# Kernel tuning notes

Measured on AMD Instinct MI355X. Metric: run time of the kernel, lower is better.

Reference implementation:

```python
import jax, jax.numpy as jnp
import numpy as np

N_NODES = 10000
N_EDGES = 640000
NODE_DIM = 128
EDGE_DIM = 32
OUT_DIM = 128


def setup_inputs() -> dict:
    key = jax.random.key(0)
    k_h, k_e, k_ef, k_w1, k_w2 = jax.random.split(key, 5)
    h = jax.random.normal(k_h, (N_NODES, NODE_DIM), dtype=jnp.float32)
    edge_index = jax.random.randint(k_e, (2, N_EDGES), 0, N_NODES, dtype=jnp.int64)
    edge_features = jax.random.normal(k_ef, (N_EDGES, EDGE_DIM), dtype=jnp.float32)
    in_dim = 2 * NODE_DIM + EDGE_DIM
    # Kaiming-ish init scale for realism
    W1 = jax.random.normal(k_w1, (in_dim, OUT_DIM), dtype=jnp.float32) / np.sqrt(in_dim)
    b1 = jnp.zeros((OUT_DIM,), dtype=jnp.float32)
    W2 = jax.random.normal(k_w2, (OUT_DIM, OUT_DIM), dtype=jnp.float32) / np.sqrt(OUT_DIM)
    b2 = jnp.zeros((OUT_DIM,), dtype=jnp.float32)
    return {"h": h, "edge_index": edge_index, "edge_features": edge_features,
            "n": N_NODES, "W1": W1, "b1": b1, "W2": W2, "b2": b2}


def reference(h, edge_index, edge_features, n, W1, b1, W2, b2):
    rows, cols = edge_index[0], edge_index[1]
    # gather source/target node features + edge features -> [E, 2*node_dim+edge_dim]
    msg_input = jnp.concatenate([h[rows], h[cols], edge_features], axis=-1)
    hidden = jax.nn.relu(msg_input @ W1 + b1)   # [E, out_dim]
    messages = hidden @ W2 + b2                 # [E, out_dim]
    # scatter-add messages onto destination rows -> [n, out_dim]
    out = jax.ops.segment_sum(messages, rows, num_segments=n)
    return out
```

## Files before the change

kernel.cpp:

```cpp
#include <hip/hip_runtime.h>
#include <hip/hip_bf16.h>


typedef __attribute__((ext_vector_type(8))) short bf16x8;
typedef __attribute__((ext_vector_type(4))) float f32x4;

#define ND 128
#define ED 32
#define CH 64

__device__ __forceinline__ short f2bf(float x) {
  unsigned int u = __float_as_uint(x);
  unsigned int r = (u + 0x7FFFu + ((u >> 16) & 1u)) >> 16;
  return (short)r;
}

__device__ __forceinline__ float bf2f(short s) {
  return __uint_as_float(((unsigned int)(unsigned short)s) << 16);
}

__device__ __forceinline__ f32x4 bf8lo(bf16x8 v) {
  f32x4 r;
  #pragma unroll
  for (int j = 0; j < 4; ++j) r[j] = bf2f(v[j]);
  return r;
}
__device__ __forceinline__ f32x4 bf8hi(bf16x8 v) {
  f32x4 r;
  #pragma unroll
  for (int j = 0; j < 4; ++j) r[j] = bf2f(v[4 + j]);
  return r;
}

__device__ __forceinline__ int load_idx(const void* ei, long long i, int is64) {
  return is64 ? (int)((const long long*)ei)[i] : ((const int*)ei)[i];
}

__device__ __forceinline__ int swz(int c) {
  int ct = c >> 4, cc = c & 15;
  return (ct >> 2) * 64 + (cc >> 2) * 16 + (ct & 3) * 4 + (cc & 3);
}

__global__ __launch_bounds__(256) void prep_kernel(
    const float* __restrict__ W1, const float* __restrict__ W2,
    const unsigned int* __restrict__ ei, short* __restrict__ w12t,
    short* __restrict__ w1eA, short* __restrict__ w2t, int* __restrict__ flag,
    int* __restrict__ counts, int N) {
  if (blockIdx.x == 0 && threadIdx.x == 0) {
    int is64 = 1;
    for (int i = 0; i < 16; ++i)
      if (ei[2 * i + 1] != 0u) is64 = 0;
    flag[0] = is64;
  }
  int t = blockIdx.x * blockDim.x + threadIdx.x;
  for (int i = t; i < N; i += 32768) counts[i] = 0;
  if (t < 256 * 128) {
    int np = t >> 7, k = t & 127;
    float v = (np < 128) ? W1[k * 128 + np] : W1[(128 + k) * 128 + (np - 128)];
    w12t[t] = f2bf(v);
  }
  if (t < 128 * 128) {
    int n = t >> 7, k = t & 127;
    w2t[t] = f2bf(W2[k * 128 + n]);
  }
  if (t < 8 * 64 * 8) {
    int ct = t >> 9, lane = (t >> 3) & 63, j = t & 7;
    int li = lane & 15, lg = lane >> 4;
    w1eA[t] = f2bf(W1[(256 + lg * 8 + j) * 128 + ct * 16 + li]);
  }
}

__global__ void hist_kernel(const void* __restrict__ ei, const int* __restrict__ flag,
                            int* __restrict__ counts, int* __restrict__ rank,
                            unsigned int* __restrict__ rc, int E) {
  int e = blockIdx.x * blockDim.x + threadIdx.x;
  if (e >= E) return;
  int f = flag[0];
  int r = load_idx(ei, e, f);
  int c = load_idx(ei, (long long)E + e, f);
  rank[e] = atomicAdd(&counts[r], 1);
  rc[e] = ((unsigned int)r << 16) | (unsigned int)c;
}

__global__ __launch_bounds__(1024) void scan_kernel(const int* __restrict__ counts,
                                                    int* __restrict__ row_ptr, int n) {
  __shared__ int wtot[16];
  int tid = threadIdx.x;
  int lane = tid & 63, w = tid >> 6;
  int base_i = tid * 16;
  int c[16];
  int tot = 0;
  #pragma unroll
  for (int j = 0; j < 16; ++j) {
    int i = base_i + j;
    c[j] = (i < n) ? counts[i] : 0;
    tot += c[j];
  }
  int x = tot;
  #pragma unroll
  for (int d = 1; d < 64; d <<= 1) {
    int t = __shfl_up(x, d);
    if (lane >= d) x += t;
  }
  if (lane == 63) wtot[w] = x;
  __syncthreads();
  if (w == 0) {
    int y = (lane < 16) ? wtot[lane] : 0;
    #pragma unroll
    for (int d = 1; d < 16; d <<= 1) {
      int t = __shfl_up(y, d);
      if (lane >= d) y += t;
    }
    if (lane < 16) wtot[lane] = y;
  }
  __syncthreads();
  int waveoff = (w == 0) ? 0 : wtot[w - 1];
  int run = waveoff + x - tot;
  if (tid == 0) row_ptr[0] = 0;
  #pragma unroll
  for (int j = 0; j < 16; ++j) {
    int i = base_i + j;
    if (i < n) {
      run += c[j];
      row_ptr[i + 1] = run;
    }
  }
}

__global__ __launch_bounds__(256, 4) void scatter_sg_kernel(
    const float* __restrict__ ef, const int* __restrict__ row_ptr,
    const int* __restrict__ rank, const unsigned int* __restrict__ rc,
    const float* __restrict__ h, const short* __restrict__ w12t,
    const float* __restrict__ b1, short* __restrict__ efb,
    unsigned short* __restrict__ ccol, int2* __restrict__ cb,
    float* __restrict__ s2, short* __restrict__ g2, int N, int E, int nchunks) {
  int b = blockIdx.x;
  int SGB = (N + 63) >> 6;
  int SCB = (4 * E + 255) >> 8;
  if (b < SGB) {
    int lane = threadIdx.x & 63, w = threadIdx.x >> 6;
    int li = lane & 15, lg = lane >> 4;
    int base = b * 64 + w * 16;
    int rowm = base + li;
    if (rowm >= N) rowm = N - 1;
    float breg[8];
    #pragma unroll
    for (int nt = 0; nt < 8; ++nt) breg[nt] = b1[nt * 16 + li];
    f32x4 acc[16];
    #pragma unroll
    for (int nt = 0; nt < 16; ++nt) acc[nt] = (f32x4){0.f, 0.f, 0.f, 0.f};
    #pragma unroll
    for (int kc = 0; kc < 4; ++kc) {
      f32x4 f0 = *(const f32x4*)(h + (size_t)rowm * ND + kc * 32 + lg * 8);
      f32x4 f1 = *(const f32x4*)(h + (size_t)rowm * ND + kc * 32 + lg * 8 + 4);
      bf16x8 a;
      #pragma unroll
      for (int j = 0; j < 4; ++j) { a[j] = f2bf(f0[j]); a[4 + j] = f2bf(f1[j]); }
      #pragma unroll
      for (int nt = 0; nt < 16; ++nt) {
        bf16x8 bb = *(const bf16x8*)(w12t + (nt * 16 + li) * 128 + kc * 32 + lg * 8);
        acc[nt] = __builtin_amdgcn_mfma_f32_16x16x32_bf16(a, bb, acc[nt], 0, 0, 0);
      }
    }
    #pragma unroll
    for (int nt = 0; nt < 16; ++nt)
      #pragma unroll
      for (int r = 0; r < 4; ++r) {
        int row = base + lg * 4 + r;
        if (row < N) {
          if (nt < 8) {
            s2[(size_t)row * 128 + swz(nt * 16 + li)] = acc[nt][r] + breg[nt];
          } else {
            g2[(size_t)row * 128 + swz((nt - 8) * 16 + li)] = f2bf(acc[nt][r]);
          }
        }
      }
  } else if (b < SGB + SCB) {
    int gt = (b - SGB) * 256 + threadIdx.x;
    int e = gt >> 2, part = gt & 3;
    if (e < E) {
      unsigned int p = rc[e];
      int r = (int)(p >> 16), c = (int)(p & 0xffffu);
      int pos = row_ptr[r] + rank[e];
      f32x4 a0 = *(const f32x4*)(ef + (size_t)e * ED + part * 8);
      f32x4 a1 = *(const f32x4*)(ef + (size_t)e * ED + part * 8 + 4);
      bf16x8 ob;
      #pragma unroll
      for (int j = 0; j < 4; ++j) { ob[j] = f2bf(a0[j]); ob[4 + j] = f2bf(a1[j]); }
      *(bf16x8*)(efb + (size_t)pos * ED + part * 8) = ob;
      if (part == 0) ccol[pos] = (unsigned short)c;
    }
  } else {
    int k = (b - SGB - SCB) * 256 + threadIdx.x;
    if (k < nchunks) {
      int t0 = k * CH, t1 = t0 + CH;
      int lo = 0, hi = N;
      while (lo < hi) { int mid = (lo + hi) >> 1; if (row_ptr[mid] < t0) lo = mid + 1; else hi = mid; }
      int na = lo;
      hi = N;
      while (lo < hi) { int mid = (lo + hi) >> 1; if (row_ptr[mid] < t1) lo = mid + 1; else hi = mid; }
      cb[k] = make_int2(na, lo);
    }
  }
}

__global__ __launch_bounds__(128, 4) void layer1_kernel(
    const float* __restrict__ s2, const short* __restrict__ g2,
    const short* __restrict__ efb, const unsigned short* __restrict__ ccol,
    const short* __restrict__ w1eA, const int* __restrict__ row_ptr,
    const int2* __restrict__ cb, float* __restrict__ hsum) {
  int2 bounds = cb[blockIdx.x];
  int na = bounds.x, nb = bounds.y;
  if (na >= nb) return;
  int lane = threadIdx.x & 63;
  int w = threadIdx.x >> 6;
  int li = lane & 15, lg = lane >> 4;

  bf16x8 wa[4];
  #pragma unroll
  for (int nt = 0; nt < 4; ++nt)
    wa[nt] = *(const bf16x8*)(w1eA + ((w * 4 + nt) * 64 + lane) * 8);

  for (int n = na; n < nb; ++n) {
    int rp = row_ptr[n], rpe = row_ptr[n + 1];
    int deg = rpe - rp;
    f32x4 sreg[4];
    #pragma unroll
    for (int nt = 0; nt < 4; ++nt)
      sreg[nt] = *(const f32x4*)(s2 + (size_t)n * 128 + w * 64 + lg * 16 + nt * 4);
    f32x4 psum[4];
    #pragma unroll
    for (int nt = 0; nt < 4; ++nt) psum[nt] = (f32x4){0.f, 0.f, 0.f, 0.f};

    int ntiles = (deg + 15) >> 4;
    int last = rpe - 1;
    auto ldpos = [&](int t) {
      int p = rp + t * 16 + li;
      return p > last ? last : p;
    };

    int pA = ldpos(0), pB = ldpos(1);
    int cA = ccol[pA], cB = ccol[pB];
    bf16x8 eA = *(const bf16x8*)(efb + (size_t)pA * ED + lg * 8);
    bf16x8 eB = *(const bf16x8*)(efb + (size_t)pB * ED + lg * 8);
    const short* gpA = g2 + (size_t)cA * 128 + w * 64 + lg * 16;
    bf16x8 gA0 = *(const bf16x8*)gpA;
    bf16x8 gA1 = *(const bf16x8*)(gpA + 8);

    for (int t = 0; t < ntiles; ++t) {
      const short* gpB = g2 + (size_t)cB * 128 + w * 64 + lg * 16;
      bf16x8 gB0 = *(const bf16x8*)gpB;
      bf16x8 gB1 = *(const bf16x8*)(gpB + 8);
      int pC = ldpos(t + 2);
      int cC = ccol[pC];
      bf16x8 eC = *(const bf16x8*)(efb + (size_t)pC * ED + lg * 8);
      f32x4 a0 = __builtin_amdgcn_mfma_f32_16x16x32_bf16(wa[0], eA, (f32x4){0.f,0.f,0.f,0.f}, 0, 0, 0);
      f32x4 a1 = __builtin_amdgcn_mfma_f32_16x16x32_bf16(wa[1], eA, (f32x4){0.f,0.f,0.f,0.f}, 0, 0, 0);
      f32x4 a2 = __builtin_amdgcn_mfma_f32_16x16x32_bf16(wa[2], eA, (f32x4){0.f,0.f,0.f,0.f}, 0, 0, 0);
      f32x4 a3 = __builtin_amdgcn_mfma_f32_16x16x32_bf16(wa[3], eA, (f32x4){0.f,0.f,0.f,0.f}, 0, 0, 0);
      if ((t * 16 + li) < deg) {
        f32x4 v0 = a0 + sreg[0] + bf8lo(gA0);
        f32x4 v1 = a1 + sreg[1] + bf8hi(gA0);
        f32x4 v2 = a2 + sreg[2] + bf8lo(gA1);
        f32x4 v3 = a3 + sreg[3] + bf8hi(gA1);
        #pragma unroll
        for (int r = 0; r < 4; ++r) {
          psum[0][r] += (v0[r] > 0.f ? v0[r] : 0.f);
          psum[1][r] += (v1[r] > 0.f ? v1[r] : 0.f);
          psum[2][r] += (v2[r] > 0.f ? v2[r] : 0.f);
          psum[3][r] += (v3[r] > 0.f ? v3[r] : 0.f);
        }
      }
      cB = cC; eA = eB; eB = eC;
      gA0 = gB0; gA1 = gB1;
    }

    #pragma unroll
    for (int nt = 0; nt < 4; ++nt)
      #pragma unroll
      for (int r = 0; r < 4; ++r) {
        float v = psum[nt][r];
        v += __shfl_xor(v, 1);
        v += __shfl_xor(v, 2);
        v += __shfl_xor(v, 4);
        v += __shfl_xor(v, 8);
        psum[nt][r] = v;
      }
    if (li == 0) {
      #pragma unroll
      for (int nt = 0; nt < 4; ++nt)
        *(f32x4*)(hsum + (size_t)n * 128 + w * 64 + nt * 16 + lg * 4) = psum[nt];
    }
  }
}

__global__ __launch_bounds__(256) void out_kernel(const float* __restrict__ hsum,
                                                  const short* __restrict__ w2t,
                                                  const float* __restrict__ b2,
                                                  const int* __restrict__ row_ptr,
                                                  float* __restrict__ out, int N) {
  int lane = threadIdx.x & 63, w = threadIdx.x >> 6;
  int li = lane & 15, lg = lane >> 4;
  int base = blockIdx.x * 64 + w * 16;
  int rowm = base + li;
  if (rowm >= N) rowm = N - 1;
  float breg[8];
  #pragma unroll
  for (int nt = 0; nt < 8; ++nt) breg[nt] = b2[nt * 16 + li];
  f32x4 acc[8];
  #pragma unroll
  for (int nt = 0; nt < 8; ++nt) acc[nt] = (f32x4){0.f, 0.f, 0.f, 0.f};
  #pragma unroll
  for (int kc = 0; kc < 4; ++kc) {
    f32x4 f0 = *(const f32x4*)(hsum + (size_t)rowm * 128 + kc * 32 + lg * 8);
    f32x4 f1 = *(const f32x4*)(hsum + (size_t)rowm * 128 + kc * 32 + lg * 8 + 4);
    bf16x8 a;
    #pragma unroll
    for (int j = 0; j < 4; ++j) { a[j] = f2bf(f0[j]); a[4 + j] = f2bf(f1[j]); }
    #pragma unroll
    for (int nt = 0; nt < 8; ++nt) {
      bf16x8 bb = *(const bf16x8*)(w2t + (nt * 16 + li) * 128 + kc * 32 + lg * 8);
      acc[nt] = __builtin_amdgcn_mfma_f32_16x16x32_bf16(a, bb, acc[nt], 0, 0, 0);
    }
  }
  #pragma unroll
  for (int r = 0; r < 4; ++r) {
    int row = base + lg * 4 + r;
    if (row < N) {
      float dg = (float)(row_ptr[row + 1] - row_ptr[row]);
      #pragma unroll
      for (int nt = 0; nt < 8; ++nt)
        out[(size_t)row * 128 + nt * 16 + li] = acc[nt][r] + dg * breg[nt];
    }
  }
}

extern "C" void kernel_launch(void* const* d_in, const int* in_sizes, int n_in,
                              void* d_out, int out_size, void* d_ws, size_t ws_size,
                              hipStream_t stream) {
  const float* h  = (const float*)d_in[0];
  const void*  ei = d_in[1];
  const float* ef = (const float*)d_in[2];
  const float* W1 = (const float*)d_in[4];
  const float* b1 = (const float*)d_in[5];
  const float* W2 = (const float*)d_in[6];
  const float* b2 = (const float*)d_in[7];
  float* out = (float*)d_out;
  int N = in_sizes[0] / ND;
  int E = in_sizes[2] / ED;
  int nchunks = (E + CH - 1) / CH;

  char* ws = (char*)d_ws;
  size_t off = 0;
  auto alloc = [&](size_t bytes) {
    size_t o = off;
    off = (off + bytes + 255) & ~(size_t)255;
    return o;
  };
  int*            flag    = (int*)(ws + alloc(4));
  int*            counts  = (int*)(ws + alloc((size_t)N * 4));
  int*            row_ptr = (int*)(ws + alloc((size_t)(N + 1) * 4));
  int*            rank    = (int*)(ws + alloc((size_t)E * 4));
  unsigned int*   rc      = (unsigned int*)(ws + alloc((size_t)E * 4));
  short*          w12t    = (short*)(ws + alloc(256 * 128 * 2));
  short*          w1eA    = (short*)(ws + alloc(8 * 64 * 8 * 2));
  short*          w2t     = (short*)(ws + alloc(128 * 128 * 2));
  float*          s2      = (float*)(ws + alloc((size_t)N * 128 * 4));
  short*          g2      = (short*)(ws + alloc((size_t)N * 128 * 2));
  float*          hsumb   = (float*)(ws + alloc((size_t)N * 128 * 4));
  short*          efb     = (short*)(ws + alloc((size_t)E * ED * 2));
  unsigned short* ccol    = (unsigned short*)(ws + alloc((size_t)E * 2));
  int2*           cbb     = (int2*)(ws + alloc((size_t)nchunks * 8));

  int SGB = (N + 63) >> 6;
  int SCB = (4 * E + 255) >> 8;
  int CBB = (nchunks + 255) >> 8;

  prep_kernel<<<128, 256, 0, stream>>>(W1, W2, (const unsigned int*)ei, w12t, w1eA, w2t,
                                       flag, counts, N);
  hist_kernel<<<(E + 255) / 256, 256, 0, stream>>>(ei, flag, counts, rank, rc, E);
  scan_kernel<<<1, 1024, 0, stream>>>(counts, row_ptr, N);
  scatter_sg_kernel<<<SGB + SCB + CBB, 256, 0, stream>>>(
      ef, row_ptr, rank, rc, h, w12t, b1, efb, ccol, cbb, s2, g2, N, E, nchunks);
  layer1_kernel<<<nchunks, 128, 0, stream>>>(s2, g2, efb, ccol, w1eA, row_ptr, cbb, hsumb);
  out_kernel<<<(N + 63) / 64, 256, 0, stream>>>(hsumb, w2t, b2, row_ptr, out, N);
}
```

Measured before the change: 139.1 us.

## Assign one layer1 block per node instead of edge-balanced chunks

Replaces edge-chunked scheduling in layer1 with one workgroup per destination node. This removes the binary-search chunk-boundary pass and the per-block node loop. The column index array widens to 32-bit ints, and the hist kernel inlines its index-width branch. In exchange, load balance now depends on the degree distribution, and ccol traffic doubles.

```diff
diff --git a/kernel.cpp b/kernel.cpp
--- a/kernel.cpp
+++ b/kernel.cpp
@@ -7,7 +7,6 @@
 
 #define ND 128
 #define ED 32
-#define CH 64
 
 __device__ __forceinline__ short f2bf(float x) {
   unsigned int u = __float_as_uint(x);
@@ -30,10 +29,6 @@
   #pragma unroll
   for (int j = 0; j < 4; ++j) r[j] = bf2f(v[4 + j]);
   return r;
-}
-
-__device__ __forceinline__ int load_idx(const void* ei, long long i, int is64) {
-  return is64 ? (int)((const long long*)ei)[i] : ((const int*)ei)[i];
 }
 
 __device__ __forceinline__ int swz(int c) {
@@ -76,8 +71,14 @@
   int e = blockIdx.x * blockDim.x + threadIdx.x;
   if (e >= E) return;
   int f = flag[0];
-  int r = load_idx(ei, e, f);
-  int c = load_idx(ei, (long long)E + e, f);
+  int r, c;
+  if (f) {
+    r = (int)((const long long*)ei)[e];
+    c = (int)((const long long*)ei)[(long long)E + e];
+  } else {
+    r = ((const int*)ei)[e];
+    c = ((const int*)ei)[E + e];
+  }
   rank[e] = atomicAdd(&counts[r], 1);
   rc[e] = ((unsigned int)r << 16) | (unsigned int)c;
 }
@@ -132,11 +133,10 @@
     const int* __restrict__ rank, const unsigned int* __restrict__ rc,
     const float* __restrict__ h, const short* __restrict__ w12t,
     const float* __restrict__ b1, short* __restrict__ efb,
-    unsigned short* __restrict__ ccol, int2* __restrict__ cb,
-    float* __restrict__ s2, short* __restrict__ g2, int N, int E, int nchunks) {
+    int* __restrict__ ccol, float* __restrict__ s2, short* __restrict__ g2,
+    int N, int E) {
   int b = blockIdx.x;
   int SGB = (N + 63) >> 6;
-  int SCB = (4 * E + 255) >> 8;
   if (b < SGB) {
     int lane = threadIdx.x & 63, w = threadIdx.x >> 6;
     int li = lane & 15, lg = lane >> 4;
@@ -175,7 +175,7 @@
           }
         }
       }
-  } else if (b < SGB + SCB) {
+  } else {
     int gt = (b - SGB) * 256 + threadIdx.x;
     int e = gt >> 2, part = gt & 3;
     if (e < E) {
@@ -188,109 +188,103 @@
       #pragma unroll
       for (int j = 0; j < 4; ++j) { ob[j] = f2bf(a0[j]); ob[4 + j] = f2bf(a1[j]); }
       *(bf16x8*)(efb + (size_t)pos * ED + part * 8) = ob;
-      if (part == 0) ccol[pos] = (unsigned short)c;
-    }
-  } else {
-    int k = (b - SGB - SCB) * 256 + threadIdx.x;
-    if (k < nchunks) {
-      int t0 = k * CH, t1 = t0 + CH;
-      int lo = 0, hi = N;
-      while (lo < hi) { int mid = (lo + hi) >> 1; if (row_ptr[mid] < t0) lo = mid + 1; else hi = mid; }
-      int na = lo;
-      hi = N;
-      while (lo < hi) { int mid = (lo + hi) >> 1; if (row_ptr[mid] < t1) lo = mid + 1; else hi = mid; }
-      cb[k] = make_int2(na, lo);
+      if (part == 0) ccol[pos] = c;
     }
   }
 }
 
 __global__ __launch_bounds__(128, 4) void layer1_kernel(
     const float* __restrict__ s2, const short* __restrict__ g2,
-    const short* __restrict__ efb, const unsigned short* __restrict__ ccol,
+    const short* __restrict__ efb, const int* __restrict__ ccol,
     const short* __restrict__ w1eA, const int* __restrict__ row_ptr,
-    const int2* __restrict__ cb, float* __restrict__ hsum) {
-  int2 bounds = cb[blockIdx.x];
-  int na = bounds.x, nb = bounds.y;
-  if (na >= nb) return;
+    float* __restrict__ hsum) {
+  int node = blockIdx.x;
   int lane = threadIdx.x & 63;
   int w = threadIdx.x >> 6;
   int li = lane & 15, lg = lane >> 4;
+  int rp = row_ptr[node], rpe = row_ptr[node + 1];
+  int deg = rpe - rp;
+
+  if (deg == 0) {
+    if (li == 0) {
+      #pragma unroll
+      for (int nt = 0; nt < 4; ++nt)
+        *(f32x4*)(hsum + (size_t)node * 128 + w * 64 + nt * 16 + lg * 4) =
+            (f32x4){0.f, 0.f, 0.f, 0.f};
+    }
+    return;
+  }
 
   bf16x8 wa[4];
   #pragma unroll
   for (int nt = 0; nt < 4; ++nt)
     wa[nt] = *(const bf16x8*)(w1eA + ((w * 4 + nt) * 64 + lane) * 8);
-
-  for (int n = na; n < nb; ++n) {
-    int rp = row_ptr[n], rpe = row_ptr[n + 1];
-    int deg = rpe - rp;
-    f32x4 sreg[4];
+  f32x4 sreg[4];
+  #pragma unroll
+  for (int nt = 0; nt < 4; ++nt)
+    sreg[nt] = *(const f32x4*)(s2 + (size_t)node * 128 + w * 64 + lg * 16 + nt * 4);
+  f32x4 psum[4];
+  #pragma unroll
+  for (int nt = 0; nt < 4; ++nt) psum[nt] = (f32x4){0.f, 0.f, 0.f, 0.f};
+
+  int ntiles = (deg + 15) >> 4;
+  int last = rpe - 1;
+  auto ldpos = [&](int t) {
+    int p = rp + t * 16 + li;
+    return p > last ? last : p;
+  };
+
+  int pA = ldpos(0), pB = ldpos(1);
+  int cA = ccol[pA], cB = ccol[pB];
+  bf16x8 eA = *(const bf16x8*)(efb + (size_t)pA * ED + lg * 8);
+  bf16x8 eB = *(const bf16x8*)(efb + (size_t)pB * ED + lg * 8);
+  const short* gpA = g2 + (size_t)cA * 128 + w * 64 + lg * 16;
+  bf16x8 gA0 = *(const bf16x8*)gpA;
+  bf16x8 gA1 = *(const bf16x8*)(gpA + 8);
+
+  for (int t = 0; t < ntiles; ++t) {
+    const short* gpB = g2 + (size_t)cB * 128 + w * 64 + lg * 16;
+    bf16x8 gB0 = *(const bf16x8*)gpB;
+    bf16x8 gB1 = *(const bf16x8*)(gpB + 8);
+    int pC = ldpos(t + 2);
+    int cC = ccol[pC];
+    bf16x8 eC = *(const bf16x8*)(efb + (size_t)pC * ED + lg * 8);
+    f32x4 a0 = __builtin_amdgcn_mfma_f32_16x16x32_bf16(wa[0], eA, (f32x4){0.f,0.f,0.f,0.f}, 0, 0, 0);
+    f32x4 a1 = __builtin_amdgcn_mfma_f32_16x16x32_bf16(wa[1], eA, (f32x4){0.f,0.f,0.f,0.f}, 0, 0, 0);
+    f32x4 a2 = __builtin_amdgcn_mfma_f32_16x16x32_bf16(wa[2], eA, (f32x4){0.f,0.f,0.f,0.f}, 0, 0, 0);
+    f32x4 a3 = __builtin_amdgcn_mfma_f32_16x16x32_bf16(wa[3], eA, (f32x4){0.f,0.f,0.f,0.f}, 0, 0, 0);
+    if ((t * 16 + li) < deg) {
+      f32x4 v0 = a0 + sreg[0] + bf8lo(gA0);
+      f32x4 v1 = a1 + sreg[1] + bf8hi(gA0);
+      f32x4 v2 = a2 + sreg[2] + bf8lo(gA1);
+      f32x4 v3 = a3 + sreg[3] + bf8hi(gA1);
+      #pragma unroll
+      for (int r = 0; r < 4; ++r) {
+        psum[0][r] += (v0[r] > 0.f ? v0[r] : 0.f);
+        psum[1][r] += (v1[r] > 0.f ? v1[r] : 0.f);
+        psum[2][r] += (v2[r] > 0.f ? v2[r] : 0.f);
+        psum[3][r] += (v3[r] > 0.f ? v3[r] : 0.f);
+      }
+    }
+    cB = cC; eA = eB; eB = eC;
+    gA0 = gB0; gA1 = gB1;
+  }
+
+  #pragma unroll
+  for (int nt = 0; nt < 4; ++nt)
+    #pragma unroll
+    for (int r = 0; r < 4; ++r) {
+      float v = psum[nt][r];
+      v += __shfl_xor(v, 1);
+      v += __shfl_xor(v, 2);
+      v += __shfl_xor(v, 4);
+      v += __shfl_xor(v, 8);
+      psum[nt][r] = v;
+    }
+  if (li == 0) {
     #pragma unroll
     for (int nt = 0; nt < 4; ++nt)
-      sreg[nt] = *(const f32x4*)(s2 + (size_t)n * 128 + w * 64 + lg * 16 + nt * 4);
-    f32x4 psum[4];
-    #pragma unroll
-    for (int nt = 0; nt < 4; ++nt) psum[nt] = (f32x4){0.f, 0.f, 0.f, 0.f};
-
-    int ntiles = (deg + 15) >> 4;
-    int last = rpe - 1;
-    auto ldpos = [&](int t) {
-      int p = rp + t * 16 + li;
-      return p > last ? last : p;
-    };
-
-    int pA = ldpos(0), pB = ldpos(1);
-    int cA = ccol[pA], cB = ccol[pB];
-    bf16x8 eA = *(const bf16x8*)(efb + (size_t)pA * ED + lg * 8);
-    bf16x8 eB = *(const bf16x8*)(efb + (size_t)pB * ED + lg * 8);
-    const short* gpA = g2 + (size_t)cA * 128 + w * 64 + lg * 16;
-    bf16x8 gA0 = *(const bf16x8*)gpA;
-    bf16x8 gA1 = *(const bf16x8*)(gpA + 8);
-
-    for (int t = 0; t < ntiles; ++t) {
-      const short* gpB = g2 + (size_t)cB * 128 + w * 64 + lg * 16;
-      bf16x8 gB0 = *(const bf16x8*)gpB;
-      bf16x8 gB1 = *(const bf16x8*)(gpB + 8);
-      int pC = ldpos(t + 2);
-      int cC = ccol[pC];
-      bf16x8 eC = *(const bf16x8*)(efb + (size_t)pC * ED + lg * 8);
-      f32x4 a0 = __builtin_amdgcn_mfma_f32_16x16x32_bf16(wa[0], eA, (f32x4){0.f,0.f,0.f,0.f}, 0, 0, 0);
-      f32x4 a1 = __builtin_amdgcn_mfma_f32_16x16x32_bf16(wa[1], eA, (f32x4){0.f,0.f,0.f,0.f}, 0, 0, 0);
-      f32x4 a2 = __builtin_amdgcn_mfma_f32_16x16x32_bf16(wa[2], eA, (f32x4){0.f,0.f,0.f,0.f}, 0, 0, 0);
-      f32x4 a3 = __builtin_amdgcn_mfma_f32_16x16x32_bf16(wa[3], eA, (f32x4){0.f,0.f,0.f,0.f}, 0, 0, 0);
-      if ((t * 16 + li) < deg) {
-        f32x4 v0 = a0 + sreg[0] + bf8lo(gA0);
-        f32x4 v1 = a1 + sreg[1] + bf8hi(gA0);
-        f32x4 v2 = a2 + sreg[2] + bf8lo(gA1);
-        f32x4 v3 = a3 + sreg[3] + bf8hi(gA1);
-        #pragma unroll
-        for (int r = 0; r < 4; ++r) {
-          psum[0][r] += (v0[r] > 0.f ? v0[r] : 0.f);
-          psum[1][r] += (v1[r] > 0.f ? v1[r] : 0.f);
-          psum[2][r] += (v2[r] > 0.f ? v2[r] : 0.f);
-          psum[3][r] += (v3[r] > 0.f ? v3[r] : 0.f);
-        }
-      }
-      cB = cC; eA = eB; eB = eC;
-      gA0 = gB0; gA1 = gB1;
-    }
-
-    #pragma unroll
-    for (int nt = 0; nt < 4; ++nt)
-      #pragma unroll
-      for (int r = 0; r < 4; ++r) {
-        float v = psum[nt][r];
-        v += __shfl_xor(v, 1);
-        v += __shfl_xor(v, 2);
-        v += __shfl_xor(v, 4);
-        v += __shfl_xor(v, 8);
-        psum[nt][r] = v;
-      }
-    if (li == 0) {
-      #pragma unroll
-      for (int nt = 0; nt < 4; ++nt)
-        *(f32x4*)(hsum + (size_t)n * 128 + w * 64 + nt * 16 + lg * 4) = psum[nt];
-    }
+      *(f32x4*)(hsum + (size_t)node * 128 + w * 64 + nt * 16 + lg * 4) = psum[nt];
   }
 }
 
@@ -348,7 +342,6 @@
   float* out = (float*)d_out;
   int N = in_sizes[0] / ND;
   int E = in_sizes[2] / ED;
-  int nchunks = (E + CH - 1) / CH;
 
   char* ws = (char*)d_ws;
   size_t off = 0;
@@ -357,31 +350,29 @@
     off = (off + bytes + 255) & ~(size_t)255;
     return o;
   };
-  int*            flag    = (int*)(ws + alloc(4));
-  int*            counts  = (int*)(ws + alloc((size_t)N * 4));
-  int*            row_ptr = (int*)(ws + alloc((size_t)(N + 1) * 4));
-  int*            rank    = (int*)(ws + alloc((size_t)E * 4));
-  unsigned int*   rc      = (unsigned int*)(ws + alloc((size_t)E * 4));
-  short*          w12t    = (short*)(ws + alloc(256 * 128 * 2));
-  short*          w1eA    = (short*)(ws + alloc(8 * 64 * 8 * 2));
-  short*          w2t     = (short*)(ws + alloc(128 * 128 * 2));
-  float*          s2      = (float*)(ws + alloc((size_t)N * 128 * 4));
-  short*          g2      = (short*)(ws + alloc((size_t)N * 128 * 2));
-  float*          hsumb   = (float*)(ws + alloc((size_t)N * 128 * 4));
-  short*          efb     = (short*)(ws + alloc((size_t)E * ED * 2));
-  unsigned short* ccol    = (unsigned short*)(ws + alloc((size_t)E * 2));
-  int2*           cbb     = (int2*)(ws + alloc((size_t)nchunks * 8));
+  int*          flag    = (int*)(ws + alloc(4));
+  int*          counts  = (int*)(ws + alloc((size_t)N * 4));
+  int*          row_ptr = (int*)(ws + alloc((size_t)(N + 1) * 4));
+  int*          rank    = (int*)(ws + alloc((size_t)E * 4));
+  unsigned int* rc      = (unsigned int*)(ws + alloc((size_t)E * 4));
+  short*        w12t    = (short*)(ws + alloc(256 * 128 * 2));
+  short*        w1eA    = (short*)(ws + alloc(8 * 64 * 8 * 2));
+  short*        w2t     = (short*)(ws + alloc(128 * 128 * 2));
+  float*        s2      = (float*)(ws + alloc((size_t)N * 128 * 4));
+  short*        g2      = (short*)(ws + alloc((size_t)N * 128 * 2));
+  float*        hsumb   = (float*)(ws + alloc((size_t)N * 128 * 4));
+  short*        efb     = (short*)(ws + alloc((size_t)E * ED * 2));
+  int*          ccol    = (int*)(ws + alloc((size_t)E * 4));
 
   int SGB = (N + 63) >> 6;
   int SCB = (4 * E + 255) >> 8;
-  int CBB = (nchunks + 255) >> 8;
 
   prep_kernel<<<128, 256, 0, stream>>>(W1, W2, (const unsigned int*)ei, w12t, w1eA, w2t,
                                        flag, counts, N);
   hist_kernel<<<(E + 255) / 256, 256, 0, stream>>>(ei, flag, counts, rank, rc, E);
   scan_kernel<<<1, 1024, 0, stream>>>(counts, row_ptr, N);
-  scatter_sg_kernel<<<SGB + SCB + CBB, 256, 0, stream>>>(
-      ef, row_ptr, rank, rc, h, w12t, b1, efb, ccol, cbb, s2, g2, N, E, nchunks);
-  layer1_kernel<<<nchunks, 128, 0, stream>>>(s2, g2, efb, ccol, w1eA, row_ptr, cbb, hsumb);
+  scatter_sg_kernel<<<SGB + SCB, 256, 0, stream>>>(
+      ef, row_ptr, rank, rc, h, w12t, b1, efb, ccol, s2, g2, N, E);
+  layer1_kernel<<<N, 128, 0, stream>>>(s2, g2, efb, ccol, w1eA, row_ptr, hsumb);
   out_kernel<<<(N + 63) / 64, 256, 0, stream>>>(hsumb, w2t, b2, row_ptr, out, N);
 }
```

Result: faster. 134.1 us (-3.6%).
